# Performance work log

Hardware: AMD Instinct MI355X
Metric: run time of the kernel (lower is better)

The kernel has to match this reference:

```python
import jax, jax.numpy as jnp
import numpy as np

N, M, D, E = 16384, 8192, 8, 2_000_000
DELTA = 1.0   # init arg delta
P = 1.0       # init arg p (forced to 1 in __init__)
EPS = 1e-6


def setup_inputs() -> dict:
    key = jax.random.key(0)
    ks = jax.random.split(key, 7)
    return {
        "gamma_rows": jax.random.normal(ks[0], (N,), dtype=jnp.float32),
        "gamma_cols": jax.random.normal(ks[1], (M,), dtype=jnp.float32),
        "latent_z": jax.random.uniform(ks[2], (N, D), dtype=jnp.float32),
        "latent_w": jax.random.uniform(ks[3], (M, D), dtype=jnp.float32),
        "weights": jax.random.uniform(ks[4], (E,), dtype=jnp.float32),
        "rows_idx": jax.random.randint(ks[5], (E,), 0, N, dtype=jnp.int32),
        "col_idx": jax.random.randint(ks[6], (E,), 0, M, dtype=jnp.int32),
    }


def reference(gamma_rows, gamma_cols, latent_z, latent_w, weights, rows_idx, col_idx):
    # Simplex projections (Softmax over latent dim)
    z = jax.nn.softmax(latent_z, axis=1)   # [N, D]
    w = jax.nn.softmax(latent_w, axis=1)   # [M, D]

    # torch.cdist(z, w, p=2): full N x M euclidean distance matrix
    sq = (jnp.sum(z * z, axis=1)[:, None]
          + jnp.sum(w * w, axis=1)[None, :]
          - 2.0 * (z @ w.T))                       # [N, M]
    dist = jnp.sqrt(jnp.maximum(sq, 0.0))          # [N, M]
    dist_matrix = -DELTA * (dist + EPS)            # [N, M]

    # z_pdist1 = exp(gamma_rows) @ exp(dist_matrix) @ exp(gamma_cols)
    z_pdist1 = jnp.einsum("i,ij,j->", jnp.exp(gamma_rows),
                          jnp.exp(dist_matrix), jnp.exp(gamma_cols))

    # Edge (link) term: per-edge euclidean distance between gathered embeddings
    delta_latent = jnp.sqrt(jnp.sum((z[rows_idx] - w[col_idx]) ** 2, axis=-1))  # [E]
    z_pdist2 = jnp.sum(weights * (gamma_rows[rows_idx] + gamma_cols[col_idx]
                                  - (DELTA * delta_latent) ** P))

    return -z_pdist2 + z_pdist1
```

## Files before the change

### kernel.cpp

```cpp
#include <hip/hip_runtime.h>
#include <math.h>

#define N_ROWS 16384
#define M_COLS 8192
#define TPB 256
#define IT 4
#define JT 64
#define JU 4
#define NJ (M_COLS / JT)
#define NIB (N_ROWS / (TPB * IT))
#define PAIR_BLOCKS (NIB * NJ)
#define EDGE_BLOCKS 1024
#define EU 8
#define GRID_BLOCKS (PAIR_BLOCKS + EDGE_BLOCKS)

typedef float v2f __attribute__((ext_vector_type(2)));
typedef _Float16 h8 __attribute__((ext_vector_type(8)));

#define C2 2.0813689810056077f
#define ROWB 32

__global__ __launch_bounds__(TPB) void rownorm_kernel(
    const float* __restrict__ lz, const float* __restrict__ gr,
    const float* __restrict__ lw, const float* __restrict__ gc,
    float* __restrict__ z, float* __restrict__ zz, float* __restrict__ eg,
    char* __restrict__ zpack,
    float* __restrict__ w, float* __restrict__ ww, float* __restrict__ ec,
    char* __restrict__ wpack)
{
    int gi = blockIdx.x * TPB + threadIdx.x;
    const float *src, *g;
    float *dv, *dq, *de;
    char* dp8;
    int i;
    if (gi < N_ROWS) { src = lz; g = gr; dv = z; dq = zz; de = eg; dp8 = zpack; i = gi; }
    else             { src = lw; g = gc; dv = w; dq = ww; de = ec; dp8 = wpack; i = gi - N_ROWS; }

    const float4* sp = (const float4*)(src + (size_t)i * 8);
    float4 a = sp[0], b = sp[1];
    float v[8] = {a.x, a.y, a.z, a.w, b.x, b.y, b.z, b.w};
    float m = v[0];
    #pragma unroll
    for (int d = 1; d < 8; d++) m = fmaxf(m, v[d]);
    float s = 0.f;
    #pragma unroll
    for (int d = 0; d < 8; d++) { v[d] = __expf(v[d] - m); s += v[d]; }
    float inv = 1.f / s;
    float sq = 0.f;
    h8 hv;
    #pragma unroll
    for (int d = 0; d < 8; d++) {
        v[d] *= inv;
        sq = fmaf(v[d], v[d], sq);
        hv[d] = (_Float16)v[d];
    }
    float gam = g[i];
    float4 o0 = {v[0], v[1], v[2], v[3]};
    float4 o1 = {v[4], v[5], v[6], v[7]};
    float4* dp = (float4*)(dv + (size_t)i * 8);
    dp[0] = o0; dp[1] = o1;
    dq[i] = C2 * sq;
    de[i] = __expf(gam);
    char* rp = dp8 + (size_t)i * ROWB;
    *(h8*)rp = hv;
    *(float*)(rp + 16) = gam;
}

__global__ __launch_bounds__(TPB) void fused_kernel(
    const float* __restrict__ z, const float* __restrict__ zz,
    const float* __restrict__ eg,
    const float* __restrict__ w, const float* __restrict__ ww,
    const float* __restrict__ ec,
    const char* __restrict__ zpack, const char* __restrict__ wpack,
    const float* __restrict__ wt,
    const int* __restrict__ ridx, const int* __restrict__ cidx, int E,
    double* __restrict__ pair_part, double* __restrict__ edge_part)
{
    __shared__ float  sw[JT * 8];
    __shared__ float  swq[JT];
    __shared__ float  sec[JT];
    __shared__ double sred[TPB];

    const int t   = threadIdx.x;
    const int bid = blockIdx.x;
    const int tri = bid / 3;
    const int rem = bid - tri * 3;

    if (rem != 0) {
        const int rid = tri * 2 + (rem - 1);
        const int ib = rid / NJ;
        const int jb = rid - ib * NJ;
        const int j0 = jb * JT;

        if (t < JT * 2) ((float4*)sw)[t] = ((const float4*)(w + (size_t)j0 * 8))[t];
        if (t < JT)     { swq[t] = ww[j0 + t]; sec[t] = ec[j0 + t]; }

        v2f  zi[IT][4];
        float zzi[IT], acc[IT];
        const int ibase = ib * (TPB * IT);
        #pragma unroll
        for (int k = 0; k < IT; k++) {
            int i = ibase + k * TPB + t;
            const float4* zp = (const float4*)(z + (size_t)i * 8);
            float4 a = zp[0], b = zp[1];
            zi[k][0] = (v2f){-2.f * C2 * a.x, -2.f * C2 * a.y};
            zi[k][1] = (v2f){-2.f * C2 * a.z, -2.f * C2 * a.w};
            zi[k][2] = (v2f){-2.f * C2 * b.x, -2.f * C2 * b.y};
            zi[k][3] = (v2f){-2.f * C2 * b.z, -2.f * C2 * b.w};
            zzi[k] = zz[i];
            acc[k] = 0.f;
        }
        __syncthreads();

        const float4* s4 = (const float4*)sw;
        for (int jo = 0; jo < JT; jo += JU) {
            float4 wa[JU], wb[JU];
            float  wq[JU], ev[JU];
            #pragma unroll
            for (int u = 0; u < JU; u++) {
                wa[u] = s4[(jo + u) * 2];
                wb[u] = s4[(jo + u) * 2 + 1];
                wq[u] = swq[jo + u];
                ev[u] = sec[jo + u];
            }
            float sq[JU][IT];
            #pragma unroll
            for (int u = 0; u < JU; u++) {
                v2f w01 = {wa[u].x, wa[u].y}, w23 = {wa[u].z, wa[u].w};
                v2f w45 = {wb[u].x, wb[u].y}, w67 = {wb[u].z, wb[u].w};
                #pragma unroll
                for (int k = 0; k < IT; k++) {
                    v2f p = zi[k][0] * w01;
                    p = __builtin_elementwise_fma(zi[k][1], w23, p);
                    p = __builtin_elementwise_fma(zi[k][2], w45, p);
                    p = __builtin_elementwise_fma(zi[k][3], w67, p);
                    sq[u][k] = fmaxf(p.x + p.y + (zzi[k] + wq[u]), 0.f);
                }
            }
            float dd[JU][IT];
            #pragma unroll
            for (int u = 0; u < JU; u++)
                #pragma unroll
                for (int k = 0; k < IT; k++)
                    asm("v_sqrt_f32 %0, %1" : "=v"(dd[u][k]) : "v"(sq[u][k]));
            float pr[JU][IT];
            #pragma unroll
            for (int u = 0; u < JU; u++)
                #pragma unroll
                for (int k = 0; k < IT; k++)
                    asm("v_exp_f32 %0, -%1" : "=v"(pr[u][k]) : "v"(dd[u][k]));
            #pragma unroll
            for (int u = 0; u < JU; u++)
                #pragma unroll
                for (int k = 0; k < IT; k++)
                    acc[k] = fmaf(ev[u], pr[u][k], acc[k]);
        }

        double tp = 0.0;
        #pragma unroll
        for (int k = 0; k < IT; k++) {
            int i = ibase + k * TPB + t;
            tp += (double)eg[i] * (double)acc[k];
        }
        sred[t] = tp;
        __syncthreads();
        for (int s = TPB / 2; s > 0; s >>= 1) {
            if (t < s) sred[t] += sred[t + s];
            __syncthreads();
        }
        if (t == 0) pair_part[rid] = sred[0];
    } else {
        const int er  = tri;
        const int tid = er * TPB + t;
        const int e0  = tid * EU;
        double local = 0.0;
        if (e0 < E) {
            int4   rr0 = *(const int4*)(ridx + e0);
            int4   rr1 = *(const int4*)(ridx + e0 + 4);
            int4   cc0 = *(const int4*)(cidx + e0);
            int4   cc1 = *(const int4*)(cidx + e0 + 4);
            float4 wtA = *(const float4*)(wt + e0);
            float4 wtB = *(const float4*)(wt + e0 + 4);
            int   r[EU]  = {rr0.x, rr0.y, rr0.z, rr0.w, rr1.x, rr1.y, rr1.z, rr1.w};
            int   c[EU]  = {cc0.x, cc0.y, cc0.z, cc0.w, cc1.x, cc1.y, cc1.z, cc1.w};
            float wv[EU] = {wtA.x, wtA.y, wtA.z, wtA.w, wtB.x, wtB.y, wtB.z, wtB.w};
            h8 zr[EU], wr[EU];
            float grv[EU], gcv[EU];
            #pragma unroll
            for (int u = 0; u < EU; u++) {
                const char* zp = zpack + (size_t)r[u] * ROWB;
                const char* wp = wpack + (size_t)c[u] * ROWB;
                zr[u]  = *(const h8*)zp;
                wr[u]  = *(const h8*)wp;
                grv[u] = *(const float*)(zp + 16);
                gcv[u] = *(const float*)(wp + 16);
            }
            #pragma unroll
            for (int u = 0; u < EU; u++) {
                h8 dv = zr[u] - wr[u];
                float s = 0.f;
                #pragma unroll
                for (int qd = 0; qd < 8; qd++) {
                    float f = (float)dv[qd];
                    s = fmaf(f, f, s);
                }
                float dist;
                asm("v_sqrt_f32 %0, %1" : "=v"(dist) : "v"(s));
                local += (double)(wv[u] * (grv[u] + gcv[u] - dist));
            }
        }
        sred[t] = local;
        __syncthreads();
        for (int s2 = TPB / 2; s2 > 0; s2 >>= 1) {
            if (t < s2) sred[t] += sred[t + s2];
            __syncthreads();
        }
        if (t == 0) edge_part[er] = sred[0];
    }
}

__global__ __launch_bounds__(TPB) void final_kernel(
    const double* __restrict__ pp, int np,
    const double* __restrict__ ep, int ne,
    float* __restrict__ out)
{
    __shared__ double sred[TPB];
    const int t = threadIdx.x;
    double s1 = 0.0, s2 = 0.0;
    for (int i = t; i < np; i += TPB) s1 += pp[i];
    for (int i = t; i < ne; i += TPB) s2 += ep[i];
    sred[t] = s1;
    __syncthreads();
    for (int s = TPB / 2; s > 0; s >>= 1) {
        if (t < s) sred[t] += sred[t + s];
        __syncthreads();
    }
    double pair_sum = sred[0];
    __syncthreads();
    sred[t] = s2;
    __syncthreads();
    for (int s = TPB / 2; s > 0; s >>= 1) {
        if (t < s) sred[t] += sred[t + s];
        __syncthreads();
    }
    if (t == 0) {
        double edge_sum = sred[0];
        double cf = exp(-1.0e-6);
        out[0] = (float)(cf * pair_sum - edge_sum);
    }
}

extern "C" void kernel_launch(void* const* d_in, const int* in_sizes, int n_in,
                              void* d_out, int out_size, void* d_ws, size_t ws_size,
                              hipStream_t stream)
{
    const float* gamma_rows = (const float*)d_in[0];
    const float* gamma_cols = (const float*)d_in[1];
    const float* latent_z   = (const float*)d_in[2];
    const float* latent_w   = (const float*)d_in[3];
    const float* weights    = (const float*)d_in[4];
    const int*   rows_idx   = (const int*)d_in[5];
    const int*   col_idx    = (const int*)d_in[6];
    float* out = (float*)d_out;
    const int E = in_sizes[4];

    char* base = (char*)d_ws;
    size_t off = 0;
    float* z  = (float*)(base + off); off += (size_t)N_ROWS * 8 * 4;
    float* zz = (float*)(base + off); off += (size_t)N_ROWS * 4;
    float* eg = (float*)(base + off); off += (size_t)N_ROWS * 4;
    float* w  = (float*)(base + off); off += (size_t)M_COLS * 8 * 4;
    float* ww = (float*)(base + off); off += (size_t)M_COLS * 4;
    float* ec = (float*)(base + off); off += (size_t)M_COLS * 4;
    char* zpack = base + off; off += (size_t)N_ROWS * ROWB;
    char* wpack = base + off; off += (size_t)M_COLS * ROWB;
    double* pair_part = (double*)(base + off); off += (size_t)PAIR_BLOCKS * 8;
    double* edge_part = (double*)(base + off); off += (size_t)EDGE_BLOCKS * 8;
    (void)ws_size;

    rownorm_kernel<<<(N_ROWS + M_COLS) / TPB, TPB, 0, stream>>>(
        latent_z, gamma_rows, latent_w, gamma_cols,
        z, zz, eg, zpack, w, ww, ec, wpack);
    fused_kernel<<<GRID_BLOCKS, TPB, 0, stream>>>(
        z, zz, eg, w, ww, ec, zpack, wpack,
        weights, rows_idx, col_idx, E, pair_part, edge_part);
    final_kernel<<<1, TPB, 0, stream>>>(pair_part, PAIR_BLOCKS,
                                        edge_part, EDGE_BLOCKS, out);
}
```

Baseline: 152.6 us.

## Compute pairwise dot products with fp16 MFMA on mean-centered embeddings

Moves the N×M cross-term from per-thread fp32 FMAs onto 16x16x32 fp16 MFMA instructions. Rows are centred by 1/D before conversion to fp16 to limit precision loss, and are zero-padded from K=8 to 32. Each wave owns a 16-row strip and a quarter of the columns, prefetching the next B fragment from global memory instead of staging in LDS. Pair and edge blocks are now interleaved 1:1. This trades fp16 rounding in the distance computation and 4x wasted MFMA K-width for fewer VALU instructions. The sqrt and exp still run per element.

```diff
diff --git a/kernel.cpp b/kernel.cpp
--- a/kernel.cpp
+++ b/kernel.cpp
@@ -4,37 +4,36 @@
 #define N_ROWS 16384
 #define M_COLS 8192
 #define TPB 256
-#define IT 4
-#define JT 64
-#define JU 4
-#define NJ (M_COLS / JT)
-#define NIB (N_ROWS / (TPB * IT))
-#define PAIR_BLOCKS (NIB * NJ)
+#define PAIR_BLOCKS 1024
 #define EDGE_BLOCKS 1024
 #define EU 8
 #define GRID_BLOCKS (PAIR_BLOCKS + EDGE_BLOCKS)
-
-typedef float v2f __attribute__((ext_vector_type(2)));
+#define JTILES 128
+
 typedef _Float16 h8 __attribute__((ext_vector_type(8)));
+typedef float f32x4 __attribute__((ext_vector_type(4)));
 
 #define C2 2.0813689810056077f
+#define MU 0.125f
 #define ROWB 32
 
 __global__ __launch_bounds__(TPB) void rownorm_kernel(
     const float* __restrict__ lz, const float* __restrict__ gr,
     const float* __restrict__ lw, const float* __restrict__ gc,
-    float* __restrict__ z, float* __restrict__ zz, float* __restrict__ eg,
+    _Float16* __restrict__ zm, float* __restrict__ szz, float* __restrict__ eg,
     char* __restrict__ zpack,
-    float* __restrict__ w, float* __restrict__ ww, float* __restrict__ ec,
+    _Float16* __restrict__ wm, float* __restrict__ sww, float* __restrict__ ec,
     char* __restrict__ wpack)
 {
     int gi = blockIdx.x * TPB + threadIdx.x;
     const float *src, *g;
-    float *dv, *dq, *de;
+    _Float16* dm;
+    float *dq, *de;
     char* dp8;
+    float ascale;
     int i;
-    if (gi < N_ROWS) { src = lz; g = gr; dv = z; dq = zz; de = eg; dp8 = zpack; i = gi; }
-    else             { src = lw; g = gc; dv = w; dq = ww; de = ec; dp8 = wpack; i = gi - N_ROWS; }
+    if (gi < N_ROWS) { src = lz; g = gr; dm = zm; dq = szz; de = eg; dp8 = zpack; ascale = -2.f * C2; i = gi; }
+    else             { src = lw; g = gc; dm = wm; dq = sww; de = ec; dp8 = wpack; ascale = 1.f;        i = gi - N_ROWS; }
 
     const float4* sp = (const float4*)(src + (size_t)i * 8);
     float4 a = sp[0], b = sp[1];
@@ -47,130 +46,101 @@
     for (int d = 0; d < 8; d++) { v[d] = __expf(v[d] - m); s += v[d]; }
     float inv = 1.f / s;
     float sq = 0.f;
-    h8 hv;
+    h8 hraw, hm;
     #pragma unroll
     for (int d = 0; d < 8; d++) {
         v[d] *= inv;
-        sq = fmaf(v[d], v[d], sq);
-        hv[d] = (_Float16)v[d];
+        hraw[d] = (_Float16)v[d];
+        float c = v[d] - MU;
+        sq = fmaf(c, c, sq);
+        hm[d] = (_Float16)(ascale * c);
     }
     float gam = g[i];
-    float4 o0 = {v[0], v[1], v[2], v[3]};
-    float4 o1 = {v[4], v[5], v[6], v[7]};
-    float4* dp = (float4*)(dv + (size_t)i * 8);
-    dp[0] = o0; dp[1] = o1;
     dq[i] = C2 * sq;
     de[i] = __expf(gam);
+    _Float16* mr = dm + (size_t)i * 32;
+    h8 zero8 = (h8)(_Float16)0.f;
+    *(h8*)mr = hm;
+    *(h8*)(mr + 8)  = zero8;
+    *(h8*)(mr + 16) = zero8;
+    *(h8*)(mr + 24) = zero8;
     char* rp = dp8 + (size_t)i * ROWB;
-    *(h8*)rp = hv;
+    *(h8*)rp = hraw;
     *(float*)(rp + 16) = gam;
 }
 
 __global__ __launch_bounds__(TPB) void fused_kernel(
-    const float* __restrict__ z, const float* __restrict__ zz,
+    const _Float16* __restrict__ zm, const float* __restrict__ szz,
     const float* __restrict__ eg,
-    const float* __restrict__ w, const float* __restrict__ ww,
+    const _Float16* __restrict__ wm, const float* __restrict__ sww,
     const float* __restrict__ ec,
     const char* __restrict__ zpack, const char* __restrict__ wpack,
     const float* __restrict__ wt,
     const int* __restrict__ ridx, const int* __restrict__ cidx, int E,
     double* __restrict__ pair_part, double* __restrict__ edge_part)
 {
-    __shared__ float  sw[JT * 8];
-    __shared__ float  swq[JT];
-    __shared__ float  sec[JT];
     __shared__ double sred[TPB];
-
     const int t   = threadIdx.x;
     const int bid = blockIdx.x;
-    const int tri = bid / 3;
-    const int rem = bid - tri * 3;
-
-    if (rem != 0) {
-        const int rid = tri * 2 + (rem - 1);
-        const int ib = rid / NJ;
-        const int jb = rid - ib * NJ;
-        const int j0 = jb * JT;
-
-        if (t < JT * 2) ((float4*)sw)[t] = ((const float4*)(w + (size_t)j0 * 8))[t];
-        if (t < JT)     { swq[t] = ww[j0 + t]; sec[t] = ec[j0 + t]; }
-
-        v2f  zi[IT][4];
-        float zzi[IT], acc[IT];
-        const int ibase = ib * (TPB * IT);
+
+    if ((bid & 1) == 0) {
+        const int lane = t & 63;
+        const int wv   = t >> 6;
+        const int gw   = (bid >> 1) * 4 + wv;
+        const int strip = gw >> 2;
+        const int jq    = gw & 3;
+        const int i0    = strip * 16;
+        const int ksl   = lane >> 4;
+        const int l15   = lane & 15;
+
+        const h8 afrag = *(const h8*)(zm + (size_t)(i0 + l15) * 32 + ksl * 8);
+        float szz4[4], eg4[4];
         #pragma unroll
-        for (int k = 0; k < IT; k++) {
-            int i = ibase + k * TPB + t;
-            const float4* zp = (const float4*)(z + (size_t)i * 8);
-            float4 a = zp[0], b = zp[1];
-            zi[k][0] = (v2f){-2.f * C2 * a.x, -2.f * C2 * a.y};
-            zi[k][1] = (v2f){-2.f * C2 * a.z, -2.f * C2 * a.w};
-            zi[k][2] = (v2f){-2.f * C2 * b.x, -2.f * C2 * b.y};
-            zi[k][3] = (v2f){-2.f * C2 * b.z, -2.f * C2 * b.w};
-            zzi[k] = zz[i];
-            acc[k] = 0.f;
-        }
-        __syncthreads();
-
-        const float4* s4 = (const float4*)sw;
-        for (int jo = 0; jo < JT; jo += JU) {
-            float4 wa[JU], wb[JU];
-            float  wq[JU], ev[JU];
+        for (int r = 0; r < 4; r++) {
+            szz4[r] = szz[i0 + 4 * ksl + r];
+            eg4[r]  = eg [i0 + 4 * ksl + r];
+        }
+
+        const f32x4 zero4 = {0.f, 0.f, 0.f, 0.f};
+        float acc = 0.f;
+
+        int j0 = jq * 2048;
+        int jcol = j0 + l15;
+        h8    bf  = *(const h8*)(wm + (size_t)jcol * 32 + ksl * 8);
+        float swl = sww[jcol];
+        float ecl = ec[jcol];
+
+        for (int jt = 0; jt < JTILES; jt++) {
+            h8 bfn; float swn, ecn;
+            if (jt < JTILES - 1) {
+                int jn = j0 + (jt + 1) * 16 + l15;
+                bfn = *(const h8*)(wm + (size_t)jn * 32 + ksl * 8);
+                swn = sww[jn];
+                ecn = ec[jn];
+            }
+            f32x4 cr = __builtin_amdgcn_mfma_f32_16x16x32_f16(afrag, bf, zero4, 0, 0, 0);
+            float s = 0.f;
             #pragma unroll
-            for (int u = 0; u < JU; u++) {
-                wa[u] = s4[(jo + u) * 2];
-                wb[u] = s4[(jo + u) * 2 + 1];
-                wq[u] = swq[jo + u];
-                ev[u] = sec[jo + u];
-            }
-            float sq[JU][IT];
-            #pragma unroll
-            for (int u = 0; u < JU; u++) {
-                v2f w01 = {wa[u].x, wa[u].y}, w23 = {wa[u].z, wa[u].w};
-                v2f w45 = {wb[u].x, wb[u].y}, w67 = {wb[u].z, wb[u].w};
-                #pragma unroll
-                for (int k = 0; k < IT; k++) {
-                    v2f p = zi[k][0] * w01;
-                    p = __builtin_elementwise_fma(zi[k][1], w23, p);
-                    p = __builtin_elementwise_fma(zi[k][2], w45, p);
-                    p = __builtin_elementwise_fma(zi[k][3], w67, p);
-                    sq[u][k] = fmaxf(p.x + p.y + (zzi[k] + wq[u]), 0.f);
-                }
-            }
-            float dd[JU][IT];
-            #pragma unroll
-            for (int u = 0; u < JU; u++)
-                #pragma unroll
-                for (int k = 0; k < IT; k++)
-                    asm("v_sqrt_f32 %0, %1" : "=v"(dd[u][k]) : "v"(sq[u][k]));
-            float pr[JU][IT];
-            #pragma unroll
-            for (int u = 0; u < JU; u++)
-                #pragma unroll
-                for (int k = 0; k < IT; k++)
-                    asm("v_exp_f32 %0, -%1" : "=v"(pr[u][k]) : "v"(dd[u][k]));
-            #pragma unroll
-            for (int u = 0; u < JU; u++)
-                #pragma unroll
-                for (int k = 0; k < IT; k++)
-                    acc[k] = fmaf(ev[u], pr[u][k], acc[k]);
-        }
-
-        double tp = 0.0;
-        #pragma unroll
-        for (int k = 0; k < IT; k++) {
-            int i = ibase + k * TPB + t;
-            tp += (double)eg[i] * (double)acc[k];
-        }
-        sred[t] = tp;
-        __syncthreads();
-        for (int s = TPB / 2; s > 0; s >>= 1) {
-            if (t < s) sred[t] += sred[t + s];
+            for (int r = 0; r < 4; r++) {
+                float vsum = fmaxf(cr[r] + szz4[r] + swl, 0.f);
+                float dd, pr;
+                asm("v_sqrt_f32 %0, %1" : "=v"(dd) : "v"(vsum));
+                asm("v_exp_f32 %0, -%1" : "=v"(pr) : "v"(dd));
+                s = fmaf(eg4[r], pr, s);
+            }
+            acc = fmaf(ecl, s, acc);
+            bf = bfn; swl = swn; ecl = ecn;
+        }
+
+        sred[t] = (double)acc;
+        __syncthreads();
+        for (int sh = TPB / 2; sh > 0; sh >>= 1) {
+            if (t < sh) sred[t] += sred[t + sh];
             __syncthreads();
         }
-        if (t == 0) pair_part[rid] = sred[0];
+        if (t == 0) pair_part[bid >> 1] = sred[0];
     } else {
-        const int er  = tri;
+        const int er  = bid >> 1;
         const int tid = er * TPB + t;
         const int e0  = tid * EU;
         double local = 0.0;
@@ -266,12 +236,12 @@
 
     char* base = (char*)d_ws;
     size_t off = 0;
-    float* z  = (float*)(base + off); off += (size_t)N_ROWS * 8 * 4;
-    float* zz = (float*)(base + off); off += (size_t)N_ROWS * 4;
-    float* eg = (float*)(base + off); off += (size_t)N_ROWS * 4;
-    float* w  = (float*)(base + off); off += (size_t)M_COLS * 8 * 4;
-    float* ww = (float*)(base + off); off += (size_t)M_COLS * 4;
-    float* ec = (float*)(base + off); off += (size_t)M_COLS * 4;
+    _Float16* zm = (_Float16*)(base + off); off += (size_t)N_ROWS * 32 * 2;
+    _Float16* wm = (_Float16*)(base + off); off += (size_t)M_COLS * 32 * 2;
+    float* szz = (float*)(base + off); off += (size_t)N_ROWS * 4;
+    float* eg  = (float*)(base + off); off += (size_t)N_ROWS * 4;
+    float* sww = (float*)(base + off); off += (size_t)M_COLS * 4;
+    float* ec  = (float*)(base + off); off += (size_t)M_COLS * 4;
     char* zpack = base + off; off += (size_t)N_ROWS * ROWB;
     char* wpack = base + off; off += (size_t)M_COLS * ROWB;
     double* pair_part = (double*)(base + off); off += (size_t)PAIR_BLOCKS * 8;
@@ -280,9 +250,9 @@
 
     rownorm_kernel<<<(N_ROWS + M_COLS) / TPB, TPB, 0, stream>>>(
         latent_z, gamma_rows, latent_w, gamma_cols,
-        z, zz, eg, zpack, w, ww, ec, wpack);
+        zm, szz, eg, zpack, wm, sww, ec, wpack);
     fused_kernel<<<GRID_BLOCKS, TPB, 0, stream>>>(
-        z, zz, eg, w, ww, ec, zpack, wpack,
+        zm, szz, eg, wm, sww, ec, zpack, wpack,
         weights, rows_idx, col_idx, E, pair_part, edge_part);
     final_kernel<<<1, TPB, 0, stream>>>(pair_part, PAIR_BLOCKS,
                                         edge_part, EDGE_BLOCKS, out);
```

After: 180.8 us. 1.18x slower.
